# Kernel optimization log

Hardware: AMD Instinct MI355X
Metric: run time of the kernel (lower is better)

Reference implementation:

```python
import jax, jax.numpy as jnp
import numpy as np

B, T, D = 2, 2048, 1024
H, Dh = 16, 64


def setup_inputs() -> dict:
    key = jax.random.key(0)
    ks = jax.random.split(key, 5)
    s = 0.02
    return {
        "x": jax.random.normal(ks[0], (B, T, D), dtype=jnp.float32),
        "attention_mask": jnp.ones((B, T), dtype=jnp.int32),
        "Wq": jax.random.normal(ks[1], (D, H * Dh), dtype=jnp.float32) * s,
        "Wk": jax.random.normal(ks[2], (D, H * Dh), dtype=jnp.float32) * s,
        "Wv": jax.random.normal(ks[3], (D, H * Dh), dtype=jnp.float32) * s,
        "Wo": jax.random.normal(ks[4], (H * Dh, D), dtype=jnp.float32) * s,
    }


def reference(x, attention_mask, Wq, Wk, Wv, Wo):
    scale = Dh ** -0.5
    # projections: [B,T,H,Dh]
    q = (x @ Wq).reshape(B, T, H, Dh)
    k = (x @ Wk).reshape(B, T, H, Dh)
    v = (x @ Wv).reshape(B, T, H, Dh)
    # scores: [B,H,T,T]
    attn = jnp.einsum("bqhd,bkhd->bhqk", q, k) * scale
    mask = attention_mask.astype(jnp.float32)[:, None, None, :]  # [B,1,1,T]
    attn = attn + (1.0 - mask) * -1e9
    attn = jax.nn.softmax(attn, axis=-1)
    # dropout p=0.0 (eval) -> identity
    out = jnp.einsum("bhqk,bkhd->bqhd", attn, v).reshape(B, T, H * Dh)
    return out @ Wo
```

## Files before the change

kernel.cpp:

```cpp
#include <hip/hip_runtime.h>
#include <stdint.h>

typedef unsigned short u16;
typedef unsigned int u32;

constexpr int CB = 2, CT = 2048, CH = 16, CDH = 64, CD = 1024;

typedef __attribute__((ext_vector_type(8))) short bf16x8;
typedef __attribute__((ext_vector_type(4))) float f32x4;
typedef __attribute__((ext_vector_type(16))) float f32x16;

typedef __attribute__((address_space(1))) const u32 as1_cu32;
typedef __attribute__((address_space(3))) u32 as3_u32;

__device__ __forceinline__ void gload_lds16(const void* g, void* l) {
  __builtin_amdgcn_global_load_lds((as1_cu32*)g, (as3_u32*)l, 16, 0, 0);
}

__device__ __forceinline__ u16 f2b(float f) {
  u32 x = __float_as_uint(f);
  u32 r = (x + 0x7fffu + ((x >> 16) & 1u)) >> 16;
  return (u16)r;
}

#if __has_builtin(__builtin_amdgcn_cvt_pk_bf16_f32)
typedef __attribute__((ext_vector_type(2))) __bf16 v2bf;
__device__ __forceinline__ u32 pk2(float a, float b) {
  v2bf r = __builtin_amdgcn_cvt_pk_bf16_f32(a, b);
  union { v2bf v; u32 u; } cv; cv.v = r; return cv.u;
}
#else
__device__ __forceinline__ u32 pk2(float a, float b) {
  return (u32)f2b(a) | ((u32)f2b(b) << 16);
}
#endif

__device__ __forceinline__ float b2f(u32 lo16) { return __uint_as_float(lo16 << 16); }

__device__ __forceinline__ float fexp2(float x) {
#if __has_builtin(__builtin_amdgcn_exp2f)
  return __builtin_amdgcn_exp2f(x);
#else
  return __expf(x * 0.69314718056f);
#endif
}

#if __has_builtin(__builtin_amdgcn_permlane32_swap)
__device__ __forceinline__ void plswap(u32& a, u32& b, int) {
  auto r = __builtin_amdgcn_permlane32_swap(a, b, false, false);
  a = (u32)r[0]; b = (u32)r[1];
}
#else
__device__ __forceinline__ void plswap(u32& a, u32& b, int hf) {
  u32 ta = (u32)__shfl_xor((int)a, 32, 64);
  u32 tb = (u32)__shfl_xor((int)b, 32, 64);
  u32 na = hf ? tb : a;
  u32 nb = hf ? b : ta;
  a = na; b = nb;
}
#endif

__global__ __launch_bounds__(256) void prep_k(const float* __restrict__ x,
                                              const float* __restrict__ Wq,
                                              const float* __restrict__ Wk,
                                              const float* __restrict__ Wv,
                                              const float* __restrict__ Wo,
                                              u16* __restrict__ Xb,
                                              u16* __restrict__ Wt) {
  __shared__ float tile[32][33];
  int bid = blockIdx.x, t = threadIdx.x;
  if (bid < 4096) {
    int i = bid * 256 + t;
    float4 v = ((const float4*)x)[i];
    ushort4 r;
    r.x = f2b(v.x); r.y = f2b(v.y); r.z = f2b(v.z); r.w = f2b(v.w);
    ((ushort4*)Xb)[i] = r;
  } else {
    int tid2 = bid - 4096;
    int mat = tid2 >> 10, b2 = tid2 & 1023;
    const float* W = (mat == 0) ? Wq : (mat == 1) ? Wk : (mat == 2) ? Wv : Wo;
    u16* dst = Wt + (size_t)mat * 1048576;
    int bx = (b2 & 31) * 32, by = (b2 >> 5) * 32;
    int tx = t & 31, ty = t >> 5;
    #pragma unroll
    for (int i = ty; i < 32; i += 8) tile[i][tx] = W[(size_t)(by + i) * CD + bx + tx];
    __syncthreads();
    #pragma unroll
    for (int i = ty; i < 32; i += 8)
      dst[(size_t)(bx + i) * CD + by + tx] = f2b(tile[tx][i]);
  }
}

__global__ __launch_bounds__(256) void gemm_qkv_k(const u16* __restrict__ A,
                                                  const u16* __restrict__ Bt,
                                                  u16* __restrict__ Cout,
                                                  int K, size_t subStride,
                                                  float scaleQ) {
  __shared__ __align__(16) u16 smem[16384];
  u16* As = smem;
  u16* Bs = smem + 8192;
  int t = threadIdx.x;
  int lane = t & 63, w = t >> 6;
  int m = lane & 15, quad = lane >> 4;
  int wrow = w >> 1, wcol = w & 1;
  int m0 = blockIdx.y * 128, n0 = blockIdx.x * 128;

  f32x4 acc[4][4];
  #pragma unroll
  for (int i = 0; i < 4; i++)
    #pragma unroll
    for (int j = 0; j < 4; j++) acc[i][j] = (f32x4){0.f, 0.f, 0.f, 0.f};

  for (int k0 = 0; k0 < K; k0 += 64) {
    __syncthreads();
    #pragma unroll
    for (int p = 0; p < 4; p++) {
      int idx = p * 256 + t;
      int row = idx >> 3, cc = (idx & 7) ^ (row & 7);
      gload_lds16(A + (size_t)(m0 + row) * K + k0 + cc * 8,
                  As + (size_t)(p * 256 + (t & 192)) * 8);
      gload_lds16(Bt + (size_t)(n0 + row) * K + k0 + cc * 8,
                  Bs + (size_t)(p * 256 + (t & 192)) * 8);
    }
    __syncthreads();
    #pragma unroll
    for (int kk = 0; kk < 2; kk++) {
      bf16x8 af[4], bfr[4];
      #pragma unroll
      for (int mt = 0; mt < 4; mt++) {
        int r = wrow * 64 + mt * 16 + m;
        af[mt] = *(const bf16x8*)&As[r * 64 + (((kk * 4 + quad) ^ (r & 7)) * 8)];
      }
      #pragma unroll
      for (int nt = 0; nt < 4; nt++) {
        int r = wcol * 64 + nt * 16 + m;
        bfr[nt] = *(const bf16x8*)&Bs[r * 64 + (((kk * 4 + quad) ^ (r & 7)) * 8)];
      }
      #pragma unroll
      for (int mt = 0; mt < 4; mt++)
        #pragma unroll
        for (int nt = 0; nt < 4; nt++)
          acc[mt][nt] = __builtin_amdgcn_mfma_f32_16x16x32_bf16(bfr[nt], af[mt],
                                                                acc[mt][nt], 0, 0, 0);
    }
  }

  float s = (n0 < 1024) ? scaleQ : 1.0f;
  __syncthreads();
  u32* Ls = (u32*)smem;
  #pragma unroll
  for (int mt = 0; mt < 4; mt++) {
    int r = wrow * 64 + mt * 16 + m;
    #pragma unroll
    for (int nt = 0; nt < 4; nt++) {
      int c = wcol * 64 + nt * 16 + quad * 4;
      uint2 pw;
      pw.x = pk2(acc[mt][nt][0] * s, acc[mt][nt][1] * s);
      pw.y = pk2(acc[mt][nt][2] * s, acc[mt][nt][3] * s);
      int chunk = c >> 3, half = (c >> 2) & 1;
      *(uint2*)(Ls + r * 64 + (((chunk ^ (r & 15)) << 2) + (half << 1))) = pw;
    }
  }
  __syncthreads();
  #pragma unroll
  for (int i = 0; i < 8; i++) {
    int row = i * 16 + (t >> 4), chunk = t & 15;
    uint4 v = *(const uint4*)(Ls + row * 64 + ((chunk ^ (row & 15)) << 2));
    int cg = n0 + chunk * 8;
    u16* outp = Cout + (size_t)(cg >> 10) * subStride + (size_t)(m0 + row) * CD + (cg & 1023);
    *(uint4*)outp = v;
  }
}

__global__ __launch_bounds__(256) void gemm_out_k(const u16* __restrict__ A,
                                                  const u16* __restrict__ Bt,
                                                  float* __restrict__ Cout, int K) {
  __shared__ __align__(16) u16 smem[16384];
  u16* As = smem;
  u16* Bs = smem + 8192;
  int t = threadIdx.x;
  int lane = t & 63, w = t >> 6;
  int m = lane & 15, quad = lane >> 4;
  int wrow = w >> 1, wcol = w & 1;
  int m0 = blockIdx.y * 128, n0 = blockIdx.x * 64;

  f32x4 acc[4][2];
  #pragma unroll
  for (int i = 0; i < 4; i++)
    #pragma unroll
    for (int j = 0; j < 2; j++) acc[i][j] = (f32x4){0.f, 0.f, 0.f, 0.f};

  for (int k0 = 0; k0 < K; k0 += 64) {
    __syncthreads();
    #pragma unroll
    for (int p = 0; p < 4; p++) {
      int idx = p * 256 + t;
      int row = idx >> 3, cc = (idx & 7) ^ (row & 7);
      gload_lds16(A + (size_t)(m0 + row) * K + k0 + cc * 8,
                  As + (size_t)(p * 256 + (t & 192)) * 8);
    }
    #pragma unroll
    for (int p = 0; p < 2; p++) {
      int idx = p * 256 + t;
      int row = idx >> 3, cc = (idx & 7) ^ (row & 7);
      gload_lds16(Bt + (size_t)(n0 + row) * K + k0 + cc * 8,
                  Bs + (size_t)(p * 256 + (t & 192)) * 8);
    }
    __syncthreads();
    #pragma unroll
    for (int kk = 0; kk < 2; kk++) {
      bf16x8 af[4], bfr[2];
      #pragma unroll
      for (int mt = 0; mt < 4; mt++) {
        int r = wrow * 64 + mt * 16 + m;
        af[mt] = *(const bf16x8*)&As[r * 64 + (((kk * 4 + quad) ^ (r & 7)) * 8)];
      }
      #pragma unroll
      for (int nt = 0; nt < 2; nt++) {
        int r = wcol * 32 + nt * 16 + m;
        bfr[nt] = *(const bf16x8*)&Bs[r * 64 + (((kk * 4 + quad) ^ (r & 7)) * 8)];
      }
      #pragma unroll
      for (int mt = 0; mt < 4; mt++)
        #pragma unroll
        for (int nt = 0; nt < 2; nt++)
          acc[mt][nt] = __builtin_amdgcn_mfma_f32_16x16x32_bf16(bfr[nt], af[mt],
                                                                acc[mt][nt], 0, 0, 0);
    }
  }

  __syncthreads();
  float* Ls = (float*)smem;
  #pragma unroll
  for (int mt = 0; mt < 4; mt++) {
    int r = wrow * 64 + mt * 16 + m;
    #pragma unroll
    for (int nt = 0; nt < 2; nt++) {
      int c = wcol * 32 + nt * 16 + quad * 4;
      int chunk = c >> 2;
      *(f32x4*)(Ls + r * 64 + ((chunk ^ (r & 15)) << 2)) = acc[mt][nt];
    }
  }
  __syncthreads();
  #pragma unroll
  for (int i = 0; i < 8; i++) {
    int row = i * 16 + (t >> 4), chunk = t & 15;
    f32x4 v = *(const f32x4*)(Ls + row * 64 + ((chunk ^ (row & 15)) << 2));
    *(f32x4*)(Cout + (size_t)(m0 + row) * CD + n0 + chunk * 4) = v;
  }
}

__global__ __launch_bounds__(256, 4) void attn_k(const u16* __restrict__ Qb,
                                                 const u16* __restrict__ Kb,
                                                 const u16* __restrict__ Vb,
                                                 const int* __restrict__ mask,
                                                 u16* __restrict__ Opart,
                                                 float* __restrict__ Lpart) {
  __shared__ __align__(16) u16 Ks[64 * 64];
  __shared__ __align__(16) u32 VsD[64 * 36];

  int t = threadIdx.x, lane = t & 63, w = t >> 6;
  int c32 = lane & 31, hf = lane >> 5;
  int qt = blockIdx.x, head = blockIdx.y;
  int b = blockIdx.z & 1, qtr = blockIdx.z >> 1;
  int kv0 = qtr * 512;
  int gid = (b * 16 + head) * 16 + qt;

  const u16* Qg = Qb + ((size_t)(b * CT + qt * 128 + w * 32 + c32)) * CD + head * CDH;
  bf16x8 qbf[4];
  #pragma unroll
  for (int kc = 0; kc < 4; kc++)
    qbf[kc] = *(const bf16x8*)(Qg + kc * 16 + hf * 8);

  const int* mk = mask + b * CT + kv0;
  int localAny = 0;
  for (int i = t; i < 512; i += 256) localAny |= (mk[i] == 0);
  int anyM = __syncthreads_or(localAny);

  f32x16 oacc[2];
  #pragma unroll
  for (int dt = 0; dt < 2; dt++)
    #pragma unroll
    for (int r = 0; r < 16; r++) oacc[dt][r] = 0.f;
  float lpA = 0.f, lpB = 0.f;

  const u16* Kg0 = Kb + ((size_t)(b * CT + kv0)) * CD + head * CDH;
  const u16* Vg0 = Vb + ((size_t)(b * CT + kv0)) * CD + head * CDH;

  int vpr = t >> 3, vdg = t & 7;
  const u16* VgT = Vg0 + (size_t)(2 * vpr) * CD + vdg * 8;
  uint4 va = *(const uint4*)VgT;
  uint4 vb2 = *(const uint4*)(VgT + CD);

  for (int kv = 0; kv < 512; kv += 64) {
    __syncthreads();
    #pragma unroll
    for (int p = 0; p < 2; p++) {
      int idx = p * 256 + t;
      int row = idx >> 3, cc = (idx & 7) ^ (row & 7);
      gload_lds16(Kg0 + (size_t)(kv + row) * CD + cc * 8,
                  Ks + (size_t)(p * 256 + (t & 192)) * 8);
    }
    {
      const u32* pa = (const u32*)&va;
      const u32* pb = (const u32*)&vb2;
      u32* dst = VsD + (size_t)vdg * 288 + (vpr ^ (vdg << 2));
      #pragma unroll
      for (int j = 0; j < 8; j++) {
        u32 lo_dw = pa[j >> 1], hi_dw = pb[j >> 1];
        u32 pkv = (j & 1) ? __builtin_amdgcn_perm(hi_dw, lo_dw, 0x07060302u)
                          : __builtin_amdgcn_perm(hi_dw, lo_dw, 0x05040100u);
        dst[j * 36] = pkv;
      }
    }
    __syncthreads();
    if (kv + 64 < 512) {
      VgT = Vg0 + (size_t)(kv + 64 + 2 * vpr) * CD + vdg * 8;
      va = *(const uint4*)VgT;
      vb2 = *(const uint4*)(VgT + CD);
    }

    #pragma unroll
    for (int kt = 0; kt < 2; kt++) {
      f32x16 sv;
      #pragma unroll
      for (int r = 0; r < 16; r++) sv[r] = 0.f;
      int key = kt * 32 + c32;
      #pragma unroll
      for (int kc = 0; kc < 4; kc++) {
        int ch = kc * 2 + hf;
        bf16x8 af = *(const bf16x8*)&Ks[key * 64 + ((ch ^ (key & 7)) * 8)];
        sv = __builtin_amdgcn_mfma_f32_32x32x16_bf16(af, qbf[kc], sv, 0, 0, 0);
      }
      u32 pk[8];
      #pragma unroll
      for (int i = 0; i < 8; i++) {
        float x0 = sv[2 * i], x1 = sv[2 * i + 1];
        if (anyM) {
          int r0 = 2 * i, r1 = 2 * i + 1;
          int mi0 = kv + kt * 32 + (r0 & 3) + 8 * (r0 >> 2) + 4 * hf;
          int mi1 = kv + kt * 32 + (r1 & 3) + 8 * (r1 >> 2) + 4 * hf;
          x0 += mk[mi0] ? 0.f : -1.0e9f;
          x1 += mk[mi1] ? 0.f : -1.0e9f;
        }
        float p0 = fexp2(x0);
        float p1 = fexp2(x1);
        lpA += p0;
        lpB += p1;
        pk[i] = pk2(p0, p1);
      }
      #pragma unroll
      for (int c = 0; c < 2; c++) {
        u32 d0 = pk[4 * c + 0], d2 = pk[4 * c + 2];
        u32 d1 = pk[4 * c + 1], d3 = pk[4 * c + 3];
        plswap(d0, d2, hf);
        plswap(d1, d3, hf);
        union { u32 u[4]; bf16x8 v; } pf;
        pf.u[0] = d0; pf.u[1] = d1; pf.u[2] = d2; pf.u[3] = d3;
        int prb = kt * 16 + c * 8 + hf * 4;
        #pragma unroll
        for (int dt = 0; dt < 2; dt++) {
          int d = dt * 32 + c32;
          const u32* vp = VsD + d * 36 + (prb ^ ((d >> 3) << 2));
          bf16x8 vf = *(const bf16x8*)vp;
          oacc[dt] = __builtin_amdgcn_mfma_f32_32x32x16_bf16(vf, pf.v, oacc[dt], 0, 0, 0);
        }
      }
    }
  }

  float lp = lpA + lpB;
  float lT = lp + __shfl_xor(lp, 32, 64);
  float linv = 1.f / lT;
  u16* Op = Opart + ((size_t)(qtr * 512 + gid) * 128 + w * 32 + c32) * 64;
  #pragma unroll
  for (int dt = 0; dt < 2; dt++) {
    #pragma unroll
    for (int g = 0; g < 4; g++) {
      float o0 = oacc[dt][4 * g + 0] * linv, o1 = oacc[dt][4 * g + 1] * linv;
      float o2 = oacc[dt][4 * g + 2] * linv, o3 = oacc[dt][4 * g + 3] * linv;
      uint2 pw;
      pw.x = pk2(o0, o1);
      pw.y = pk2(o2, o3);
      *(uint2*)(Op + dt * 32 + 8 * g + 4 * hf) = pw;
    }
  }
  if (lane < 32) Lpart[(size_t)(qtr * 512 + gid) * 128 + w * 32 + lane] = lT;
}

__global__ __launch_bounds__(256) void combine_k(const u16* __restrict__ Opart,
                                                 const float* __restrict__ Lpart,
                                                 u16* __restrict__ Ob) {
  int fid = blockIdx.x * 256 + threadIdx.x;
  int gid = fid >> 11;
  int rem = fid & 2047;
  int r = rem >> 4, d = (rem & 15) * 4;
  int b = gid >> 8, head = (gid >> 4) & 15, qt = gid & 15;
  float l[4], lsum = 0.f;
  uint2 A[4];
  #pragma unroll
  for (int q = 0; q < 4; q++) {
    size_t idx = (size_t)(q * 512 + gid) * 128 + r;
    l[q] = Lpart[idx];
    A[q] = *(const uint2*)(Opart + idx * 64 + d);
    lsum += l[q];
  }
  float inv = 1.f / lsum;
  float o0 = 0.f, o1 = 0.f, o2 = 0.f, o3 = 0.f;
  #pragma unroll
  for (int q = 0; q < 4; q++) {
    float wq = l[q] * inv;
    o0 += wq * b2f(A[q].x & 0xffffu);
    o1 += wq * b2f(A[q].x >> 16);
    o2 += wq * b2f(A[q].y & 0xffffu);
    o3 += wq * b2f(A[q].y >> 16);
  }
  uint2 pw;
  pw.x = pk2(o0, o1);
  pw.y = pk2(o2, o3);
  size_t trow = (size_t)b * CT + qt * 128 + r;
  *(uint2*)(Ob + trow * CD + head * CDH + d) = pw;
}

extern "C" void kernel_launch(void* const* d_in, const int* in_sizes, int n_in,
                              void* d_out, int out_size, void* d_ws, size_t ws_size,
                              hipStream_t stream) {
  const float* x  = (const float*)d_in[0];
  const int* mask = (const int*)d_in[1];
  const float* Wq = (const float*)d_in[2];
  const float* Wk = (const float*)d_in[3];
  const float* Wv = (const float*)d_in[4];
  const float* Wo = (const float*)d_in[5];
  float* out = (float*)d_out;

  u16* Xb    = (u16*)d_ws;
  u16* Wqkv  = Xb + (size_t)4096 * 1024;
  u16* WoT   = Wqkv + (size_t)3072 * 1024;
  u16* Qb    = Wqkv + (size_t)4096 * 1024;
  u16* Ob    = Qb + (size_t)3 * 4096 * 1024;
  u16* Opart = Ob + (size_t)4096 * 1024;
  float* Lpart = (float*)(Opart + (size_t)4 * 512 * 128 * 64);

  const float EC = 0.18033688f;

  prep_k<<<8192, 256, 0, stream>>>(x, Wq, Wk, Wv, Wo, Xb, Wqkv);
  gemm_qkv_k<<<dim3(24, 32), 256, 0, stream>>>(Xb, Wqkv, Qb, 1024,
                                               (size_t)4096 * 1024, EC);
  attn_k<<<dim3(16, 16, 8), 256, 0, stream>>>(Qb, Qb + (size_t)4096 * 1024,
                                              Qb + (size_t)2 * 4096 * 1024, mask,
                                              Opart, Lpart);
  combine_k<<<4096, 256, 0, stream>>>(Opart, Lpart, Ob);
  gemm_out_k<<<dim3(16, 32), 256, 0, stream>>>(Ob, WoT, out, 1024);
}
```

Before: 203.4 us.

## Process two 32-row query groups per wave to reuse K/V LDS fragments

Each wave now handles 64 query rows instead of 32, so every K fragment and V fragment read from shared memory feeds two MFMAs. The attention grid shrinks from 16 to 8 query tiles per head, and the partial-output layout and combine indexing change to match. The aim is to halve the LDS reads and the K/V staging per query row. The cost is higher register pressure (launch bounds drop from 4 to 3 waves) and half as many blocks (1024), which may leave CUs less well filled.

```diff
diff --git a/kernel.cpp b/kernel.cpp
--- a/kernel.cpp
+++ b/kernel.cpp
@@ -250,7 +250,7 @@
   }
 }
 
-__global__ __launch_bounds__(256, 4) void attn_k(const u16* __restrict__ Qb,
+__global__ __launch_bounds__(256, 3) void attn_k(const u16* __restrict__ Qb,
                                                  const u16* __restrict__ Kb,
                                                  const u16* __restrict__ Vb,
                                                  const int* __restrict__ mask,
@@ -264,25 +264,30 @@
   int qt = blockIdx.x, head = blockIdx.y;
   int b = blockIdx.z & 1, qtr = blockIdx.z >> 1;
   int kv0 = qtr * 512;
-  int gid = (b * 16 + head) * 16 + qt;
-
-  const u16* Qg = Qb + ((size_t)(b * CT + qt * 128 + w * 32 + c32)) * CD + head * CDH;
-  bf16x8 qbf[4];
-  #pragma unroll
-  for (int kc = 0; kc < 4; kc++)
-    qbf[kc] = *(const bf16x8*)(Qg + kc * 16 + hf * 8);
+  int gid = (b * 16 + head) * 8 + qt;
+
+  bf16x8 qbf[2][4];
+  #pragma unroll
+  for (int qg = 0; qg < 2; qg++) {
+    const u16* Qg = Qb + ((size_t)(b * CT + qt * 256 + w * 64 + qg * 32 + c32)) * CD + head * CDH;
+    #pragma unroll
+    for (int kc = 0; kc < 4; kc++)
+      qbf[qg][kc] = *(const bf16x8*)(Qg + kc * 16 + hf * 8);
+  }
 
   const int* mk = mask + b * CT + kv0;
   int localAny = 0;
   for (int i = t; i < 512; i += 256) localAny |= (mk[i] == 0);
   int anyM = __syncthreads_or(localAny);
 
-  f32x16 oacc[2];
-  #pragma unroll
-  for (int dt = 0; dt < 2; dt++)
-    #pragma unroll
-    for (int r = 0; r < 16; r++) oacc[dt][r] = 0.f;
-  float lpA = 0.f, lpB = 0.f;
+  f32x16 oacc[2][2];
+  #pragma unroll
+  for (int qg = 0; qg < 2; qg++)
+    #pragma unroll
+    for (int dt = 0; dt < 2; dt++)
+      #pragma unroll
+      for (int r = 0; r < 16; r++) oacc[qg][dt][r] = 0.f;
+  float lpA[2] = {0.f, 0.f}, lpB[2] = {0.f, 0.f};
 
   const u16* Kg0 = Kb + ((size_t)(b * CT + kv0)) * CD + head * CDH;
   const u16* Vg0 = Vb + ((size_t)(b * CT + kv0)) * CD + head * CDH;
@@ -322,85 +327,102 @@
 
     #pragma unroll
     for (int kt = 0; kt < 2; kt++) {
-      f32x16 sv;
-      #pragma unroll
-      for (int r = 0; r < 16; r++) sv[r] = 0.f;
+      bf16x8 af[4];
       int key = kt * 32 + c32;
       #pragma unroll
-      for (int kc = 0; kc < 4; kc++) {
-        int ch = kc * 2 + hf;
-        bf16x8 af = *(const bf16x8*)&Ks[key * 64 + ((ch ^ (key & 7)) * 8)];
-        sv = __builtin_amdgcn_mfma_f32_32x32x16_bf16(af, qbf[kc], sv, 0, 0, 0);
-      }
-      u32 pk[8];
-      #pragma unroll
-      for (int i = 0; i < 8; i++) {
-        float x0 = sv[2 * i], x1 = sv[2 * i + 1];
-        if (anyM) {
-          int r0 = 2 * i, r1 = 2 * i + 1;
-          int mi0 = kv + kt * 32 + (r0 & 3) + 8 * (r0 >> 2) + 4 * hf;
-          int mi1 = kv + kt * 32 + (r1 & 3) + 8 * (r1 >> 2) + 4 * hf;
-          x0 += mk[mi0] ? 0.f : -1.0e9f;
-          x1 += mk[mi1] ? 0.f : -1.0e9f;
+      for (int kc = 0; kc < 4; kc++)
+        af[kc] = *(const bf16x8*)&Ks[key * 64 + (((kc * 2 + hf) ^ (key & 7)) * 8)];
+
+      u32 pfr[2][2][4];
+      #pragma unroll
+      for (int qg = 0; qg < 2; qg++) {
+        f32x16 sv;
+        #pragma unroll
+        for (int r = 0; r < 16; r++) sv[r] = 0.f;
+        #pragma unroll
+        for (int kc = 0; kc < 4; kc++)
+          sv = __builtin_amdgcn_mfma_f32_32x32x16_bf16(af[kc], qbf[qg][kc], sv, 0, 0, 0);
+        u32 pk[8];
+        #pragma unroll
+        for (int i = 0; i < 8; i++) {
+          float x0 = sv[2 * i], x1 = sv[2 * i + 1];
+          if (anyM) {
+            int r0 = 2 * i, r1 = 2 * i + 1;
+            int mi0 = kv + kt * 32 + (r0 & 3) + 8 * (r0 >> 2) + 4 * hf;
+            int mi1 = kv + kt * 32 + (r1 & 3) + 8 * (r1 >> 2) + 4 * hf;
+            x0 += mk[mi0] ? 0.f : -1.0e9f;
+            x1 += mk[mi1] ? 0.f : -1.0e9f;
+          }
+          float p0 = fexp2(x0);
+          float p1 = fexp2(x1);
+          lpA[qg] += p0;
+          lpB[qg] += p1;
+          pk[i] = pk2(p0, p1);
         }
-        float p0 = fexp2(x0);
-        float p1 = fexp2(x1);
-        lpA += p0;
-        lpB += p1;
-        pk[i] = pk2(p0, p1);
+        #pragma unroll
+        for (int c = 0; c < 2; c++) {
+          u32 d0 = pk[4 * c + 0], d2 = pk[4 * c + 2];
+          u32 d1 = pk[4 * c + 1], d3 = pk[4 * c + 3];
+          plswap(d0, d2, hf);
+          plswap(d1, d3, hf);
+          pfr[qg][c][0] = d0; pfr[qg][c][1] = d1;
+          pfr[qg][c][2] = d2; pfr[qg][c][3] = d3;
+        }
       }
       #pragma unroll
       for (int c = 0; c < 2; c++) {
-        u32 d0 = pk[4 * c + 0], d2 = pk[4 * c + 2];
-        u32 d1 = pk[4 * c + 1], d3 = pk[4 * c + 3];
-        plswap(d0, d2, hf);
-        plswap(d1, d3, hf);
-        union { u32 u[4]; bf16x8 v; } pf;
-        pf.u[0] = d0; pf.u[1] = d1; pf.u[2] = d2; pf.u[3] = d3;
         int prb = kt * 16 + c * 8 + hf * 4;
         #pragma unroll
         for (int dt = 0; dt < 2; dt++) {
           int d = dt * 32 + c32;
-          const u32* vp = VsD + d * 36 + (prb ^ ((d >> 3) << 2));
-          bf16x8 vf = *(const bf16x8*)vp;
-          oacc[dt] = __builtin_amdgcn_mfma_f32_32x32x16_bf16(vf, pf.v, oacc[dt], 0, 0, 0);
+          bf16x8 vf = *(const bf16x8*)(VsD + d * 36 + (prb ^ ((d >> 3) << 2)));
+          union { u32 u[4]; bf16x8 v; } pf0, pf1;
+          #pragma unroll
+          for (int q2 = 0; q2 < 4; q2++) { pf0.u[q2] = pfr[0][c][q2]; pf1.u[q2] = pfr[1][c][q2]; }
+          oacc[0][dt] = __builtin_amdgcn_mfma_f32_32x32x16_bf16(vf, pf0.v, oacc[0][dt], 0, 0, 0);
+          oacc[1][dt] = __builtin_amdgcn_mfma_f32_32x32x16_bf16(vf, pf1.v, oacc[1][dt], 0, 0, 0);
         }
       }
     }
   }
 
-  float lp = lpA + lpB;
-  float lT = lp + __shfl_xor(lp, 32, 64);
-  float linv = 1.f / lT;
-  u16* Op = Opart + ((size_t)(qtr * 512 + gid) * 128 + w * 32 + c32) * 64;
-  #pragma unroll
-  for (int dt = 0; dt < 2; dt++) {
-    #pragma unroll
-    for (int g = 0; g < 4; g++) {
-      float o0 = oacc[dt][4 * g + 0] * linv, o1 = oacc[dt][4 * g + 1] * linv;
-      float o2 = oacc[dt][4 * g + 2] * linv, o3 = oacc[dt][4 * g + 3] * linv;
-      uint2 pw;
-      pw.x = pk2(o0, o1);
-      pw.y = pk2(o2, o3);
-      *(uint2*)(Op + dt * 32 + 8 * g + 4 * hf) = pw;
-    }
-  }
-  if (lane < 32) Lpart[(size_t)(qtr * 512 + gid) * 128 + w * 32 + lane] = lT;
+  #pragma unroll
+  for (int qg = 0; qg < 2; qg++) {
+    float lp = lpA[qg] + lpB[qg];
+    float lT = lp + __shfl_xor(lp, 32, 64);
+    float linv = 1.f / lT;
+    int row = w * 64 + qg * 32 + c32;
+    u16* Op = Opart + ((size_t)(qtr * 256 + gid) * 256 + row) * 64;
+    #pragma unroll
+    for (int dt = 0; dt < 2; dt++) {
+      #pragma unroll
+      for (int g = 0; g < 4; g++) {
+        float o0 = oacc[qg][dt][4 * g + 0] * linv, o1 = oacc[qg][dt][4 * g + 1] * linv;
+        float o2 = oacc[qg][dt][4 * g + 2] * linv, o3 = oacc[qg][dt][4 * g + 3] * linv;
+        uint2 pw;
+        pw.x = pk2(o0, o1);
+        pw.y = pk2(o2, o3);
+        *(uint2*)(Op + dt * 32 + 8 * g + 4 * hf) = pw;
+      }
+    }
+    if (hf == 0)
+      Lpart[(size_t)(qtr * 256 + gid) * 256 + row] = lT;
+  }
 }
 
 __global__ __launch_bounds__(256) void combine_k(const u16* __restrict__ Opart,
                                                  const float* __restrict__ Lpart,
                                                  u16* __restrict__ Ob) {
   int fid = blockIdx.x * 256 + threadIdx.x;
-  int gid = fid >> 11;
-  int rem = fid & 2047;
+  int gid = fid >> 12;
+  int rem = fid & 4095;
   int r = rem >> 4, d = (rem & 15) * 4;
-  int b = gid >> 8, head = (gid >> 4) & 15, qt = gid & 15;
+  int b = gid >> 7, head = (gid >> 3) & 15, qt = gid & 7;
   float l[4], lsum = 0.f;
   uint2 A[4];
   #pragma unroll
   for (int q = 0; q < 4; q++) {
-    size_t idx = (size_t)(q * 512 + gid) * 128 + r;
+    size_t idx = (size_t)(q * 256 + gid) * 256 + r;
     l[q] = Lpart[idx];
     A[q] = *(const uint2*)(Opart + idx * 64 + d);
     lsum += l[q];
@@ -418,7 +440,7 @@
   uint2 pw;
   pw.x = pk2(o0, o1);
   pw.y = pk2(o2, o3);
-  size_t trow = (size_t)b * CT + qt * 128 + r;
+  size_t trow = (size_t)b * CT + qt * 256 + r;
   *(uint2*)(Ob + trow * CD + head * CDH + d) = pw;
 }
 
@@ -439,16 +461,16 @@
   u16* Qb    = Wqkv + (size_t)4096 * 1024;
   u16* Ob    = Qb + (size_t)3 * 4096 * 1024;
   u16* Opart = Ob + (size_t)4096 * 1024;
-  float* Lpart = (float*)(Opart + (size_t)4 * 512 * 128 * 64);
+  float* Lpart = (float*)(Opart + (size_t)4 * 256 * 256 * 64);
 
   const float EC = 0.18033688f;
 
   prep_k<<<8192, 256, 0, stream>>>(x, Wq, Wk, Wv, Wo, Xb, Wqkv);
   gemm_qkv_k<<<dim3(24, 32), 256, 0, stream>>>(Xb, Wqkv, Qb, 1024,
                                                (size_t)4096 * 1024, EC);
-  attn_k<<<dim3(16, 16, 8), 256, 0, stream>>>(Qb, Qb + (size_t)4096 * 1024,
-                                              Qb + (size_t)2 * 4096 * 1024, mask,
-                                              Opart, Lpart);
+  attn_k<<<dim3(8, 16, 8), 256, 0, stream>>>(Qb, Qb + (size_t)4096 * 1024,
+                                             Qb + (size_t)2 * 4096 * 1024, mask,
+                                             Opart, Lpart);
   combine_k<<<4096, 256, 0, stream>>>(Opart, Lpart, Ob);
   gemm_out_k<<<dim3(16, 32), 256, 0, stream>>>(Ob, WoT, out, 1024);
 }
```

New measurement: 314.4 us. 1.55x slower.
